# Optimization experiments

Measured on AMD Instinct MI355X. Metric: run time of the kernel, lower is better.

The kernel has to match this reference:

```python
import jax, jax.numpy as jnp
import numpy as np

RES = 64          # img_resolution
SIGMA = 1.0       # Gaussian kernel sigma
PI = RES * RES    # flattened persistence image size
B, P0, P1 = 256, 1024, 512
EPS_P = 1e-6
EPS_D = 1e-8
LN_EPS = 1e-5


def setup_inputs() -> dict:
    key = jax.random.key(0)
    ks = jax.random.split(key, 8)
    pairs_h0 = jax.random.uniform(ks[0], (B, P0, 2), dtype=jnp.float32)
    pairs_h1 = jax.random.uniform(ks[1], (B, P1, 2), dtype=jnp.float32)
    W1 = jax.random.normal(ks[2], (2 * PI, 512), dtype=jnp.float32) * 0.02
    W2 = jax.random.normal(ks[3], (512, 256), dtype=jnp.float32) * 0.02
    W3 = jax.random.normal(ks[4], (256, 128), dtype=jnp.float32) * 0.02
    return dict(
        pairs_h0=pairs_h0, pairs_h1=pairs_h1,
        W1=W1, b1=jnp.zeros((512,), jnp.float32), g1=jnp.ones((512,), jnp.float32), be1=jnp.zeros((512,), jnp.float32),
        W2=W2, b2=jnp.zeros((256,), jnp.float32), g2=jnp.ones((256,), jnp.float32), be2=jnp.zeros((256,), jnp.float32),
        W3=W3, b3=jnp.zeros((128,), jnp.float32),
    )


def _masked_minmax(x, valid):
    big = jnp.float32(1e30)
    mn = jnp.min(jnp.where(valid, x, big))
    mx = jnp.max(jnp.where(valid, x, -big))
    degen = (mx - mn) < 1e-6
    mn = jnp.where(degen, 0.0, mn)
    mx = jnp.where(degen, 1.0, mx)
    return mn, mx


def _pers_image(pairs):
    """pairs: [P, 2] (birth, death) -> [RES, RES] persistence image."""
    births = pairs[:, 0]
    pers = pairs[:, 1] - pairs[:, 0]
    valid = pers > EPS_P
    any_valid = jnp.any(valid)
    bmin, bmax = _masked_minmax(births, valid)
    pmin, pmax = _masked_minmax(pers, valid)
    bn = (births - bmin) / (bmax - bmin + EPS_D)   # [P]
    pn = (pers - pmin) / (pmax - pmin + EPS_D)     # [P]
    w = jnp.where(valid, pers, 0.0)                # weight = persistence, invalid -> 0
    grid = jnp.linspace(0.0, 1.0, RES)
    inv2s2 = 1.0 / (2.0 * SIGMA * SIGMA)
    kb = jnp.exp(-((grid[None, :] - bn[:, None]) ** 2) * inv2s2)  # [P, RES] over b_grid
    kp = jnp.exp(-((grid[None, :] - pn[:, None]) ** 2) * inv2s2)  # [P, RES] over p_grid
    # img[i, j] = sum_p w_p * exp(-(bdiff_p[i] + pdiff_p[j]) / 2s^2)  (separable Gaussian)
    img = jnp.einsum('p,pi,pj->ij', w, kb, kp)
    return jnp.where(any_valid, img, jnp.zeros_like(img))


def _layernorm(x, g, b):
    mu = jnp.mean(x, axis=-1, keepdims=True)
    var = jnp.mean((x - mu) ** 2, axis=-1, keepdims=True)
    return (x - mu) * jax.lax.rsqrt(var + LN_EPS) * g + b


def reference(pairs_h0, pairs_h1, W1, b1, g1, be1, W2, b2, g2, be2, W3, b3):
    bsz = pairs_h0.shape[0]
    pi0 = jax.vmap(_pers_image)(pairs_h0).reshape(bsz, -1)  # [B, RES*RES]
    pi1 = jax.vmap(_pers_image)(pairs_h1).reshape(bsz, -1)
    feats = jnp.concatenate([pi0, pi1], axis=1)             # [B, 2*PI]
    h = jax.nn.relu(_layernorm(feats @ W1 + b1, g1, be1))   # dropout: eval mode (identity)
    h = jax.nn.relu(_layernorm(h @ W2 + b2, g2, be2))
    return h @ W3 + b3
```

## Files before the change

kernel.cpp:

```cpp
#include <hip/hip_runtime.h>
#include <hip/hip_bf16.h>
#include <hip/hip_fp16.h>


#define P0_N 1024
#define P1_N 512

typedef _Float16 h2 __attribute__((ext_vector_type(2)));
typedef _Float16 f16x8 __attribute__((ext_vector_type(8)));
typedef float f32x4 __attribute__((ext_vector_type(4)));

#define KSCALE 0.849321804f
#define DG (KSCALE / 63.0f)

static __device__ __forceinline__ float fast_exp2(float x) {
#if defined(__has_builtin)
#if __has_builtin(__builtin_amdgcn_exp2f)
    return __builtin_amdgcn_exp2f(x);
#else
    return exp2f(x);
#endif
#else
    return exp2f(x);
#endif
}

__global__ __launch_bounds__(256) void pi_kernel(const float* __restrict__ p0,
                                                 const float* __restrict__ p1,
                                                 _Float16* __restrict__ featsH)
{
    const int task = blockIdx.x;
    const int b    = task >> 1;
    const int hom  = task & 1;
    const int P    = hom ? P1_N : P0_N;
    const float* pairs = hom ? (p1 + (size_t)b * P1_N * 2)
                             : (p0 + (size_t)b * P0_N * 2);
    const int t = threadIdx.x;
    const int w = t >> 6, lane = t & 63;

    __shared__ float cbs[1024], cps[1024], cws[1024];
    __shared__ __align__(16) _Float16 kbT[64][72];
    __shared__ __align__(16) _Float16 kpT[64][72];
    __shared__ float wmn0[4], wmx0[4], wmn1[4], wmx1[4];
    __shared__ unsigned gcnt[16];

    float bv_[4], pv_[4];
    bool  val[4];
    float bmin = 1e30f, bmax = -1e30f, pmin = 1e30f, pmax = -1e30f;
    #pragma unroll
    for (int s = 0; s < 4; ++s) {
        const int p = t + s * 256;
        val[s] = false; bv_[s] = 0.0f; pv_[s] = 0.0f;
        if (p < P) {
            const float2 pr = ((const float2*)pairs)[p];
            const float birth = pr.x;
            const float pers  = pr.y - pr.x;
            bv_[s] = birth; pv_[s] = pers;
            val[s] = pers > 1e-6f;
            if (val[s]) {
                bmin = fminf(bmin, birth); bmax = fmaxf(bmax, birth);
                pmin = fminf(pmin, pers);  pmax = fmaxf(pmax, pers);
            }
        }
    }
    #pragma unroll
    for (int d = 32; d > 0; d >>= 1) {
        bmin = fminf(bmin, __shfl_xor(bmin, d));
        bmax = fmaxf(bmax, __shfl_xor(bmax, d));
        pmin = fminf(pmin, __shfl_xor(pmin, d));
        pmax = fmaxf(pmax, __shfl_xor(pmax, d));
    }
    unsigned long long msk[4];
    #pragma unroll
    for (int s = 0; s < 4; ++s) msk[s] = __ballot(val[s]);
    if (lane == 0) {
        wmn0[w] = bmin; wmx0[w] = bmax; wmn1[w] = pmin; wmx1[w] = pmax;
        #pragma unroll
        for (int s = 0; s < 4; ++s) gcnt[w * 4 + s] = (unsigned)__popcll(msk[s]);
    }
    __syncthreads();
    float bmn = fminf(fminf(wmn0[0], wmn0[1]), fminf(wmn0[2], wmn0[3]));
    float bmx = fmaxf(fmaxf(wmx0[0], wmx0[1]), fmaxf(wmx0[2], wmx0[3]));
    float pmn = fminf(fminf(wmn1[0], wmn1[1]), fminf(wmn1[2], wmn1[3]));
    float pmx = fmaxf(fmaxf(wmx1[0], wmx1[1]), fmaxf(wmx1[2], wmx1[3]));
    if (bmx - bmn < 1e-6f) { bmn = 0.0f; bmx = 1.0f; }
    if (pmx - pmn < 1e-6f) { pmn = 0.0f; pmx = 1.0f; }
    const float binv = KSCALE / (bmx - bmn + 1e-8f);
    const float pinv = KSCALE / (pmx - pmn + 1e-8f);

    unsigned gb[4] = {0, 0, 0, 0};
    unsigned run = 0;
    #pragma unroll
    for (int g = 0; g < 16; ++g) {
        #pragma unroll
        for (int s = 0; s < 4; ++s)
            if (g == w * 4 + s) gb[s] = run;
        run += gcnt[g];
    }
    const int nv = (int)run;
    const int nchunks = (nv + 63) >> 6;

    const unsigned long long below = (1ull << lane) - 1ull;
    #pragma unroll
    for (int s = 0; s < 4; ++s) {
        if (val[s]) {
            const unsigned pos = gb[s] + (unsigned)__popcll(msk[s] & below);
            cbs[pos] = (bv_[s] - bmn) * binv;
            cps[pos] = (pv_[s] - pmn) * pinv;
            cws[pos] = pv_[s];
        }
    }
    for (int i = nv + t; i < nchunks * 64; i += 256) {
        cbs[i] = 0.0f; cps[i] = 0.0f; cws[i] = 0.0f;
    }

    const int pp   = lane & 31;
    const int surf = lane >> 5;
    const int c0   = w * 16;
    const float Gq = (float)c0 * DG;
    const float rho = fast_exp2(-2.0f * DG * DG);
    const float c1  = -DG * DG * (float)(2 * c0 + 1);
    const float* Xarr = surf ? cps : cbs;
    _Float16* surfT = surf ? &kpT[0][0] : &kbT[0][0];

    const int wm = (w >> 1) * 32, wn = (w & 1) * 32;
    const int fr = lane & 15, fg = lane >> 4;

    f32x4 acc[2][2] = {};

    for (int c = 0; c < nchunks; ++c) {
        const int base = c * 64;
        __syncthreads();
        const float X0 = Xarr[base + 2 * pp];
        const float X1 = Xarr[base + 2 * pp + 1];
        float W0 = 1.0f, W1 = 1.0f;
        if (!surf) { W0 = cws[base + 2 * pp]; W1 = cws[base + 2 * pp + 1]; }
        const float d0 = Gq - X0, d1 = Gq - X1;
        float v0 = W0 * fast_exp2(-(d0 * d0));
        float v1 = W1 * fast_exp2(-(d1 * d1));
        float r0 = fast_exp2(c1 + 2.0f * DG * X0);
        float r1 = fast_exp2(c1 + 2.0f * DG * X1);
        #pragma unroll
        for (int j = 0; j < 16; ++j) {
            h2 hv; hv[0] = (_Float16)v0; hv[1] = (_Float16)v1;
            *(h2*)&surfT[(c0 + j) * 72 + 2 * pp] = hv;
            v0 *= r0; r0 *= rho;
            v1 *= r1; r1 *= rho;
        }
        __syncthreads();
        #pragma unroll
        for (int ks2 = 0; ks2 < 64; ks2 += 32) {
            f16x8 af[2], bf[2];
            af[0] = *(const f16x8*)&kbT[wm + fr][ks2 + fg * 8];
            af[1] = *(const f16x8*)&kbT[wm + 16 + fr][ks2 + fg * 8];
            bf[0] = *(const f16x8*)&kpT[wn + fr][ks2 + fg * 8];
            bf[1] = *(const f16x8*)&kpT[wn + 16 + fr][ks2 + fg * 8];
            #pragma unroll
            for (int i = 0; i < 2; ++i)
                #pragma unroll
                for (int j = 0; j < 2; ++j)
                    acc[i][j] = __builtin_amdgcn_mfma_f32_16x16x32_f16(
                        af[i], bf[j], acc[i][j], 0, 0, 0);
        }
    }

    _Float16* dst = featsH + (size_t)b * 8192 + hom * 4096;
    #pragma unroll
    for (int i = 0; i < 2; ++i)
        #pragma unroll
        for (int j = 0; j < 2; ++j) {
            const int r0_ = wm + i * 16 + fg * 4;
            const int cc  = wn + j * 16 + fr;
            #pragma unroll
            for (int r = 0; r < 4; ++r)
                dst[(size_t)(r0_ + r) * 64 + cc] = (_Float16)acc[i][j][r];
        }
}

__global__ __launch_bounds__(256) void gemm1_mfma(const _Float16* __restrict__ Ah,
                                                  const float* __restrict__ W1,
                                                  float* __restrict__ part)
{
    const int mt = blockIdx.x;
    const int nt = blockIdx.y;
    const int ks = blockIdx.z;
    const int t  = threadIdx.x;

    __shared__ _Float16 As[64][72];
    __shared__ _Float16 Bs[64][72];

    const int mbase = mt * 64, nbase = nt * 64, kbase = ks * 512;
    const int lrow = t >> 2, lk0 = (t & 3) * 16;
    const int kr   = t >> 2, c0  = (t & 3) * 16;

    const _Float16* Ap = Ah + (size_t)(mbase + lrow) * 8192 + kbase + lk0;
    const float*    Wp = W1 + (size_t)(kbase + kr) * 512 + nbase + c0;

    const int w = t >> 6, lane = t & 63;
    const int wm = (w >> 1) * 32, wn = (w & 1) * 32;
    const int fr = lane & 15, fg = lane >> 4;

    f32x4 acc[2][2] = {};

    uint4  pa0 = *(const uint4*)(Ap);
    uint4  pa1 = *(const uint4*)(Ap + 8);
    float4 pw0 = *(const float4*)(Wp);
    float4 pw1 = *(const float4*)(Wp + 4);
    float4 pw2 = *(const float4*)(Wp + 8);
    float4 pw3 = *(const float4*)(Wp + 12);

    for (int k0 = 0; k0 < 512; k0 += 64) {
        __syncthreads();
        *(uint4*)&As[lrow][lk0]     = pa0;
        *(uint4*)&As[lrow][lk0 + 8] = pa1;
        {
            const float wv[16] = { pw0.x, pw0.y, pw0.z, pw0.w,
                                   pw1.x, pw1.y, pw1.z, pw1.w,
                                   pw2.x, pw2.y, pw2.z, pw2.w,
                                   pw3.x, pw3.y, pw3.z, pw3.w };
            #pragma unroll
            for (int j = 0; j < 16; ++j) Bs[c0 + j][kr] = (_Float16)wv[j];
        }
        __syncthreads();
        if (k0 + 64 < 512) {
            pa0 = *(const uint4*)(Ap + k0 + 64);
            pa1 = *(const uint4*)(Ap + k0 + 72);
            const float* wn_ = Wp + (size_t)(k0 + 64) * 512;
            pw0 = *(const float4*)(wn_);
            pw1 = *(const float4*)(wn_ + 4);
            pw2 = *(const float4*)(wn_ + 8);
            pw3 = *(const float4*)(wn_ + 12);
        }
        #pragma unroll
        for (int ks2 = 0; ks2 < 64; ks2 += 32) {
            f16x8 af[2], bf[2];
            af[0] = *(const f16x8*)&As[wm + fr][ks2 + fg * 8];
            af[1] = *(const f16x8*)&As[wm + 16 + fr][ks2 + fg * 8];
            bf[0] = *(const f16x8*)&Bs[wn + fr][ks2 + fg * 8];
            bf[1] = *(const f16x8*)&Bs[wn + 16 + fr][ks2 + fg * 8];
            #pragma unroll
            for (int i = 0; i < 2; ++i)
                #pragma unroll
                for (int j = 0; j < 2; ++j)
                    acc[i][j] = __builtin_amdgcn_mfma_f32_16x16x32_f16(
                        af[i], bf[j], acc[i][j], 0, 0, 0);
        }
    }

    #pragma unroll
    for (int i = 0; i < 2; ++i)
        #pragma unroll
        for (int j = 0; j < 2; ++j) {
            const int r0 = mbase + wm + i * 16 + fg * 4;
            const int c  = nbase + wn + j * 16 + fr;
            float* dst = part + (size_t)ks * (256 * 512) + (size_t)r0 * 512 + c;
            #pragma unroll
            for (int r = 0; r < 4; ++r) dst[(size_t)r * 512] = acc[i][j][r];
        }
}

__global__ __launch_bounds__(1024) void tail_kernel(const float* __restrict__ part,
    const float* __restrict__ b1, const float* __restrict__ g1, const float* __restrict__ be1,
    const float* __restrict__ W2, const float* __restrict__ b2, const float* __restrict__ g2, const float* __restrict__ be2,
    const float* __restrict__ W3, const float* __restrict__ b3,
    float* __restrict__ out)
{
    const int row  = blockIdx.x;
    const int t    = threadIdx.x;
    const int wid  = t >> 6, lane = t & 63;

    __shared__ float h1s[512];
    __shared__ float h2s[256];
    __shared__ float red[1024];
    __shared__ __align__(16) float red4[1024][4];
    __shared__ float wredA[16], wredB[16];

    const int col = t & 511, sb8 = (t >> 9) * 8;
    float v = 0.0f;
    #pragma unroll
    for (int s = 0; s < 8; ++s)
        v += part[(size_t)(sb8 + s) * (256 * 512) + (size_t)row * 512 + col];
    red[t] = v;
    __syncthreads();
    float x = 0.0f;
    if (t < 512) x = red[t] + red[t + 512] + b1[col];

    float s1 = (t < 512) ? x : 0.0f;
    float s2 = (t < 512) ? x * x : 0.0f;
    #pragma unroll
    for (int d = 32; d > 0; d >>= 1) {
        s1 += __shfl_xor(s1, d);
        s2 += __shfl_xor(s2, d);
    }
    if (lane == 0) { wredA[wid] = s1; wredB[wid] = s2; }
    __syncthreads();
    float mu = 0.0f, m2 = 0.0f;
    #pragma unroll
    for (int i = 0; i < 16; ++i) { mu += wredA[i]; m2 += wredB[i]; }
    mu *= (1.0f / 512.0f);
    m2  = m2 * (1.0f / 512.0f) - mu * mu;
    const float rs = rsqrtf(m2 + 1e-5f);
    if (t < 512) h1s[col] = fmaxf((x - mu) * rs * g1[col] + be1[col], 0.0f);
    __syncthreads();

    const int cg2 = t & 63, ksl = t >> 6;
    {
        float4 a4 = make_float4(0.0f, 0.0f, 0.0f, 0.0f);
        const float* w2p = W2 + (size_t)(ksl * 32) * 256 + cg2 * 4;
        const float* h1p = h1s + ksl * 32;
        #pragma unroll 8
        for (int k = 0; k < 32; ++k) {
            const float4 wv = *(const float4*)(w2p + (size_t)k * 256);
            const float hv = h1p[k];
            a4.x += hv * wv.x; a4.y += hv * wv.y;
            a4.z += hv * wv.z; a4.w += hv * wv.w;
        }
        *(float4*)red4[t] = a4;
    }
    __syncthreads();
    float y = 0.0f;
    if (t < 256) {
        const float* r4f = (const float*)red4;
        const int base = (t >> 2) * 4 + (t & 3);
        #pragma unroll
        for (int s = 0; s < 16; ++s) y += r4f[s * 256 + base];
        y += b2[t];
    }

    s1 = (t < 256) ? y : 0.0f;
    s2 = (t < 256) ? y * y : 0.0f;
    #pragma unroll
    for (int d = 32; d > 0; d >>= 1) {
        s1 += __shfl_xor(s1, d);
        s2 += __shfl_xor(s2, d);
    }
    if (lane == 0) { wredA[wid] = s1; wredB[wid] = s2; }
    __syncthreads();
    mu = 0.0f; m2 = 0.0f;
    #pragma unroll
    for (int i = 0; i < 16; ++i) { mu += wredA[i]; m2 += wredB[i]; }
    mu *= (1.0f / 256.0f);
    m2  = m2 * (1.0f / 256.0f) - mu * mu;
    const float rs2 = rsqrtf(m2 + 1e-5f);
    if (t < 256) h2s[t] = fmaxf((y - mu) * rs2 * g2[t] + be2[t], 0.0f);
    __syncthreads();

    const int col3 = t & 127, ks3 = t >> 7;
    float o = 0.0f;
    #pragma unroll 8
    for (int k = 0; k < 32; ++k)
        o += h2s[ks3 * 32 + k] * W3[(size_t)(ks3 * 32 + k) * 128 + col3];
    red[t] = o;
    __syncthreads();
    if (t < 128) {
        float oo = 0.0f;
        #pragma unroll
        for (int s = 0; s < 8; ++s) oo += red[t + s * 128];
        out[(size_t)row * 128 + t] = oo + b3[t];
    }
}

extern "C" void kernel_launch(void* const* d_in, const int* in_sizes, int n_in,
                              void* d_out, int out_size, void* d_ws, size_t ws_size,
                              hipStream_t stream)
{
    const float* p0  = (const float*)d_in[0];
    const float* p1  = (const float*)d_in[1];
    const float* W1  = (const float*)d_in[2];
    const float* b1  = (const float*)d_in[3];
    const float* g1  = (const float*)d_in[4];
    const float* be1 = (const float*)d_in[5];
    const float* W2  = (const float*)d_in[6];
    const float* b2  = (const float*)d_in[7];
    const float* g2  = (const float*)d_in[8];
    const float* be2 = (const float*)d_in[9];
    const float* W3  = (const float*)d_in[10];
    const float* b3  = (const float*)d_in[11];
    float* out = (float*)d_out;

    _Float16* featsH = (_Float16*)d_ws;
    float*    part   = (float*)((char*)d_ws + (4u << 20));

    hipLaunchKernelGGL(pi_kernel,    dim3(512),      dim3(256),  0, stream, p0, p1, featsH);
    hipLaunchKernelGGL(gemm1_mfma,   dim3(4, 8, 16), dim3(256),  0, stream, featsH, W1, part);
    hipLaunchKernelGGL(tail_kernel,  dim3(256),      dim3(1024), 0, stream, part,
                       b1, g1, be1, W2, b2, g2, be2, W3, b3, out);
}
```

Measured before the change: 42.21 us.

## Double-buffer PI kernel chunks, double split-K, and pack W1 fp16 conversion

The persistence-image kernel now double-buffers its Gaussian kernel tiles in shared memory. It generates chunk c+1 while running MFMAs on chunk c, which removes one barrier per chunk. The first GEMM doubles its split-K factor from 16 to 32 so more blocks run, and the tail kernel sums 32 partials instead of 16. W1 tiles are now loaded as four rows and converted with packed round-toward-zero f16 conversion and 8-byte shared stores, replacing 16 scalar transposed stores. The trade-offs are more shared memory per block, extra partial-sum traffic, and a slight rounding difference from RTZ conversion.

```diff
diff --git a/kernel.cpp b/kernel.cpp
--- a/kernel.cpp
+++ b/kernel.cpp
@@ -22,6 +22,18 @@
 #endif
 #else
     return exp2f(x);
+#endif
+}
+
+static __device__ __forceinline__ h2 pk2(float a, float b) {
+#if defined(__has_builtin)
+#if __has_builtin(__builtin_amdgcn_cvt_pkrtz)
+    return __builtin_bit_cast(h2, __builtin_amdgcn_cvt_pkrtz(a, b));
+#else
+    h2 r; r[0] = (_Float16)a; r[1] = (_Float16)b; return r;
+#endif
+#else
+    h2 r; r[0] = (_Float16)a; r[1] = (_Float16)b; return r;
 #endif
 }
 
@@ -39,8 +51,8 @@
     const int w = t >> 6, lane = t & 63;
 
     __shared__ float cbs[1024], cps[1024], cws[1024];
-    __shared__ __align__(16) _Float16 kbT[64][72];
-    __shared__ __align__(16) _Float16 kpT[64][72];
+    __shared__ __align__(16) _Float16 kbT[2][64][72];
+    __shared__ __align__(16) _Float16 kpT[2][64][72];
     __shared__ float wmn0[4], wmx0[4], wmn1[4], wmx1[4];
     __shared__ unsigned gcnt[16];
 
@@ -117,20 +129,18 @@
     const int pp   = lane & 31;
     const int surf = lane >> 5;
     const int c0   = w * 16;
-    const float Gq = (float)c0 * DG;
+    const float Gq  = (float)c0 * DG;
     const float rho = fast_exp2(-2.0f * DG * DG);
     const float c1  = -DG * DG * (float)(2 * c0 + 1);
     const float* Xarr = surf ? cps : cbs;
-    _Float16* surfT = surf ? &kpT[0][0] : &kbT[0][0];
 
     const int wm = (w >> 1) * 32, wn = (w & 1) * 32;
     const int fr = lane & 15, fg = lane >> 4;
 
     f32x4 acc[2][2] = {};
 
-    for (int c = 0; c < nchunks; ++c) {
+    auto gen_chunk = [&](int c, int bi) {
         const int base = c * 64;
-        __syncthreads();
         const float X0 = Xarr[base + 2 * pp];
         const float X1 = Xarr[base + 2 * pp + 1];
         float W0 = 1.0f, W1 = 1.0f;
@@ -140,21 +150,22 @@
         float v1 = W1 * fast_exp2(-(d1 * d1));
         float r0 = fast_exp2(c1 + 2.0f * DG * X0);
         float r1 = fast_exp2(c1 + 2.0f * DG * X1);
+        _Float16* sT = surf ? &kpT[bi][0][0] : &kbT[bi][0][0];
         #pragma unroll
         for (int j = 0; j < 16; ++j) {
-            h2 hv; hv[0] = (_Float16)v0; hv[1] = (_Float16)v1;
-            *(h2*)&surfT[(c0 + j) * 72 + 2 * pp] = hv;
+            *(h2*)&sT[(c0 + j) * 72 + 2 * pp] = pk2(v0, v1);
             v0 *= r0; r0 *= rho;
             v1 *= r1; r1 *= rho;
         }
-        __syncthreads();
+    };
+    auto consume_chunk = [&](int bi) {
         #pragma unroll
         for (int ks2 = 0; ks2 < 64; ks2 += 32) {
             f16x8 af[2], bf[2];
-            af[0] = *(const f16x8*)&kbT[wm + fr][ks2 + fg * 8];
-            af[1] = *(const f16x8*)&kbT[wm + 16 + fr][ks2 + fg * 8];
-            bf[0] = *(const f16x8*)&kpT[wn + fr][ks2 + fg * 8];
-            bf[1] = *(const f16x8*)&kpT[wn + 16 + fr][ks2 + fg * 8];
+            af[0] = *(const f16x8*)&kbT[bi][wm + fr][ks2 + fg * 8];
+            af[1] = *(const f16x8*)&kbT[bi][wm + 16 + fr][ks2 + fg * 8];
+            bf[0] = *(const f16x8*)&kpT[bi][wn + fr][ks2 + fg * 8];
+            bf[1] = *(const f16x8*)&kpT[bi][wn + 16 + fr][ks2 + fg * 8];
             #pragma unroll
             for (int i = 0; i < 2; ++i)
                 #pragma unroll
@@ -162,6 +173,15 @@
                     acc[i][j] = __builtin_amdgcn_mfma_f32_16x16x32_f16(
                         af[i], bf[j], acc[i][j], 0, 0, 0);
         }
+    };
+
+    __syncthreads();
+    if (nchunks > 0) gen_chunk(0, 0);
+    __syncthreads();
+    for (int c = 0; c < nchunks; ++c) {
+        if (c + 1 < nchunks) gen_chunk(c + 1, (c + 1) & 1);
+        consume_chunk(c & 1);
+        __syncthreads();
     }
 
     _Float16* dst = featsH + (size_t)b * 8192 + hom * 4096;
@@ -189,12 +209,12 @@
     __shared__ _Float16 As[64][72];
     __shared__ _Float16 Bs[64][72];
 
-    const int mbase = mt * 64, nbase = nt * 64, kbase = ks * 512;
+    const int mbase = mt * 64, nbase = nt * 64, kbase = ks * 256;
     const int lrow = t >> 2, lk0 = (t & 3) * 16;
-    const int kr   = t >> 2, c0  = (t & 3) * 16;
+    const int k0s  = (t >> 4) * 4, nc = (t & 15) * 4;
 
     const _Float16* Ap = Ah + (size_t)(mbase + lrow) * 8192 + kbase + lk0;
-    const float*    Wp = W1 + (size_t)(kbase + kr) * 512 + nbase + c0;
+    const float*    Wp = W1 + (size_t)(kbase + k0s) * 512 + nbase + nc;
 
     const int w = t >> 6, lane = t & 63;
     const int wm = (w >> 1) * 32, wn = (w & 1) * 32;
@@ -205,31 +225,34 @@
     uint4  pa0 = *(const uint4*)(Ap);
     uint4  pa1 = *(const uint4*)(Ap + 8);
     float4 pw0 = *(const float4*)(Wp);
-    float4 pw1 = *(const float4*)(Wp + 4);
-    float4 pw2 = *(const float4*)(Wp + 8);
-    float4 pw3 = *(const float4*)(Wp + 12);
-
-    for (int k0 = 0; k0 < 512; k0 += 64) {
+    float4 pw1 = *(const float4*)(Wp + 512);
+    float4 pw2 = *(const float4*)(Wp + 1024);
+    float4 pw3 = *(const float4*)(Wp + 1536);
+
+    for (int k0 = 0; k0 < 256; k0 += 64) {
         __syncthreads();
         *(uint4*)&As[lrow][lk0]     = pa0;
         *(uint4*)&As[lrow][lk0 + 8] = pa1;
         {
-            const float wv[16] = { pw0.x, pw0.y, pw0.z, pw0.w,
-                                   pw1.x, pw1.y, pw1.z, pw1.w,
-                                   pw2.x, pw2.y, pw2.z, pw2.w,
-                                   pw3.x, pw3.y, pw3.z, pw3.w };
-            #pragma unroll
-            for (int j = 0; j < 16; ++j) Bs[c0 + j][kr] = (_Float16)wv[j];
+            union { uint2 u; h2 h[2]; } pk;
+            pk.h[0] = pk2(pw0.x, pw1.x); pk.h[1] = pk2(pw2.x, pw3.x);
+            *(uint2*)&Bs[nc + 0][k0s] = pk.u;
+            pk.h[0] = pk2(pw0.y, pw1.y); pk.h[1] = pk2(pw2.y, pw3.y);
+            *(uint2*)&Bs[nc + 1][k0s] = pk.u;
+            pk.h[0] = pk2(pw0.z, pw1.z); pk.h[1] = pk2(pw2.z, pw3.z);
+            *(uint2*)&Bs[nc + 2][k0s] = pk.u;
+            pk.h[0] = pk2(pw0.w, pw1.w); pk.h[1] = pk2(pw2.w, pw3.w);
+            *(uint2*)&Bs[nc + 3][k0s] = pk.u;
         }
         __syncthreads();
-        if (k0 + 64 < 512) {
+        if (k0 + 64 < 256) {
             pa0 = *(const uint4*)(Ap + k0 + 64);
             pa1 = *(const uint4*)(Ap + k0 + 72);
             const float* wn_ = Wp + (size_t)(k0 + 64) * 512;
             pw0 = *(const float4*)(wn_);
-            pw1 = *(const float4*)(wn_ + 4);
-            pw2 = *(const float4*)(wn_ + 8);
-            pw3 = *(const float4*)(wn_ + 12);
+            pw1 = *(const float4*)(wn_ + 512);
+            pw2 = *(const float4*)(wn_ + 1024);
+            pw3 = *(const float4*)(wn_ + 1536);
         }
         #pragma unroll
         for (int ks2 = 0; ks2 < 64; ks2 += 32) {
@@ -275,11 +298,11 @@
     __shared__ __align__(16) float red4[1024][4];
     __shared__ float wredA[16], wredB[16];
 
-    const int col = t & 511, sb8 = (t >> 9) * 8;
+    const int col = t & 511, sb16 = (t >> 9) * 16;
     float v = 0.0f;
     #pragma unroll
-    for (int s = 0; s < 8; ++s)
-        v += part[(size_t)(sb8 + s) * (256 * 512) + (size_t)row * 512 + col];
+    for (int s = 0; s < 16; ++s)
+        v += part[(size_t)(sb16 + s) * (256 * 512) + (size_t)row * 512 + col];
     red[t] = v;
     __syncthreads();
     float x = 0.0f;
@@ -382,7 +405,7 @@
     float*    part   = (float*)((char*)d_ws + (4u << 20));
 
     hipLaunchKernelGGL(pi_kernel,    dim3(512),      dim3(256),  0, stream, p0, p1, featsH);
-    hipLaunchKernelGGL(gemm1_mfma,   dim3(4, 8, 16), dim3(256),  0, stream, featsH, W1, part);
+    hipLaunchKernelGGL(gemm1_mfma,   dim3(4, 8, 32), dim3(256),  0, stream, featsH, W1, part);
     hipLaunchKernelGGL(tail_kernel,  dim3(256),      dim3(1024), 0, stream, part,
                        b1, g1, be1, W2, b2, g2, be2, W3, b3, out);
 }
```

Result: slower. 43.61 us (+3.3%).
